# Optimization experiments

Hardware: AMD Instinct MI355X
Metric: run time of the kernel (lower is better)

The kernel has to match this reference:

```python
import jax, jax.numpy as jnp
import numpy as np

A = 512   # input channels
B = 32    # number of capsule types
H4 = 16   # h*h pose dims per capsule


def setup_inputs() -> dict:
    key = jax.random.key(0)
    k1, k2, k3, k4, k5 = jax.random.split(key, 5)
    # Input feature map [N, A, H, W]
    x = jax.random.normal(k1, (64, A, 32, 32), dtype=jnp.float32)
    # Fused weights: B parallel 1x1 convs concatenated along out-channel dim.
    # Pose convs: B x Conv2d(A -> 16, k=1) -> [B*16, A]; activation convs: B x Conv2d(A -> 1) -> [B, A]
    bound = 1.0 / np.sqrt(A)  # PyTorch Conv2d default init range
    W_pose = jax.random.uniform(k2, (B * H4, A), minval=-bound, maxval=bound, dtype=jnp.float32)
    b_pose = jax.random.uniform(k3, (B * H4,), minval=-bound, maxval=bound, dtype=jnp.float32)
    W_act = jax.random.uniform(k4, (B, A), minval=-bound, maxval=bound, dtype=jnp.float32)
    b_act = jax.random.uniform(k5, (B,), minval=-bound, maxval=bound, dtype=jnp.float32)
    return {"x": x, "W_pose": W_pose, "b_pose": b_pose, "W_act": W_act, "b_act": b_act}


def reference(x, W_pose, b_pose, W_act, b_act):
    # 1x1 conv == channel contraction; fuse all 2*B tiny convs into two GEMMs.
    # poses: [N, B*16, H, W]
    poses = jnp.einsum('nahw,oa->nohw', x, W_pose) + b_pose[None, :, None, None]
    # activations: sigmoid([N, B, H, W])
    activations = jax.nn.sigmoid(jnp.einsum('nahw,oa->nohw', x, W_act) + b_act[None, :, None, None])
    return poses, activations
```

## Files before the change

### kernel.cpp

```cpp
#include <hip/hip_runtime.h>
#include <hip/hip_bf16.h>


typedef __attribute__((ext_vector_type(8))) short short8;
typedef __attribute__((ext_vector_type(4))) float f32x4;

#define A_CH   512
#define HW     1024
#define N_B    64
#define O_POSE 512
#define O_ACT  32
#define O_TOT  544
#define TILE   128
#define BK     32

__device__ __forceinline__ unsigned pack_bf16x2(float lo, float hi) {
    __hip_bfloat162 h = __float22bfloat162_rn(make_float2(lo, hi));
    return *reinterpret_cast<unsigned*>(&h);
}

__global__ __launch_bounds__(256) void caps_fused_gemm(
    const float* __restrict__ x,
    const float* __restrict__ Wp,
    const float* __restrict__ bp,
    const float* __restrict__ Wa,
    const float* __restrict__ ba,
    float* __restrict__ out)
{
    __shared__ __align__(16) short ldsA[TILE * BK];
    __shared__ __align__(16) short ldsB[TILE * BK];

    const int tid = threadIdx.x;
    const int n   = blockIdx.z;
    const int o0  = blockIdx.y * TILE;
    const int m0  = blockIdx.x * TILE;

    const float* xn = x + (size_t)n * A_CH * HW + m0;

    const int bm  = tid & 127;
    const int bkh = (tid >> 7) * 16;

    float4 a_reg[4];
    float  b_reg[4][4];

    auto load_tiles = [&](int k0) {
#pragma unroll
        for (int c = 0; c < 4; ++c) {
            int lin = tid + 256 * c;
            int o = lin >> 3, kc = lin & 7;
            int R = o0 + o;
            float4 v = make_float4(0.f, 0.f, 0.f, 0.f);
            if (R < O_POSE)     v = *(const float4*)(Wp + (size_t)R * A_CH + k0 + kc * 4);
            else if (R < O_TOT) v = *(const float4*)(Wa + (size_t)(R - O_POSE) * A_CH + k0 + kc * 4);
            a_reg[c] = v;
        }
#pragma unroll
        for (int c = 0; c < 4; ++c) {
            int kb = k0 + bkh + c * 4;
#pragma unroll
            for (int j = 0; j < 4; ++j)
                b_reg[c][j] = xn[(size_t)(kb + j) * HW + bm];
        }
    };

    auto store_tiles = [&]() {
#pragma unroll
        for (int c = 0; c < 4; ++c) {
            int lin = tid + 256 * c;
            int o = lin >> 3, kc = lin & 7;
            int kx = (kc * 4) ^ (8 * ((o >> 1) & 3));
            uint2 p;
            p.x = pack_bf16x2(a_reg[c].x, a_reg[c].y);
            p.y = pack_bf16x2(a_reg[c].z, a_reg[c].w);
            *(uint2*)&ldsA[o * BK + kx] = p;
        }
#pragma unroll
        for (int c = 0; c < 4; ++c) {
            int kloc = bkh + c * 4;
            int kx = kloc ^ (8 * ((bm >> 1) & 3));
            uint2 p;
            p.x = pack_bf16x2(b_reg[c][0], b_reg[c][1]);
            p.y = pack_bf16x2(b_reg[c][2], b_reg[c][3]);
            *(uint2*)&ldsB[bm * BK + kx] = p;
        }
    };

    const int lane = tid & 63;
    const int w    = tid >> 6;
    const int wo   = (w >> 1) * 64;
    const int wm   = (w & 1) * 64;
    const int l16  = lane & 15;
    const int g    = lane >> 4;

    f32x4 acc[4][4] = {};

    load_tiles(0);

    for (int it = 0; it < A_CH / BK; ++it) {
        __syncthreads();
        store_tiles();
        __syncthreads();
        if (it + 1 < A_CH / BK) load_tiles((it + 1) * BK);

        short8 aF[4], bF[4];
#pragma unroll
        for (int f = 0; f < 4; ++f) {
            int r  = wo + f * 16 + l16;
            int kx = (g * 8) ^ (8 * ((r >> 1) & 3));
            aF[f] = *(const short8*)&ldsA[r * BK + kx];
            int cC  = wm + f * 16 + l16;
            int kxb = (g * 8) ^ (8 * ((cC >> 1) & 3));
            bF[f] = *(const short8*)&ldsB[cC * BK + kxb];
        }
#pragma unroll
        for (int fo = 0; fo < 4; ++fo)
#pragma unroll
            for (int fm = 0; fm < 4; ++fm)
                acc[fo][fm] = __builtin_amdgcn_mfma_f32_16x16x32_bf16(
                    aF[fo], bF[fm], acc[fo][fm], 0, 0, 0);
    }

    float* actOut = out + (size_t)N_B * O_POSE * HW;
    const size_t poseN = (size_t)n * O_POSE * HW;
    const size_t actN  = (size_t)n * O_ACT * HW;
#pragma unroll
    for (int fo = 0; fo < 4; ++fo) {
#pragma unroll
        for (int i = 0; i < 4; ++i) {
            int R = o0 + wo + fo * 16 + g * 4 + i;
            if (R >= O_TOT) continue;
            if (R < O_POSE) {
                float bias = bp[R];
#pragma unroll
                for (int fm = 0; fm < 4; ++fm) {
                    int cc = m0 + wm + fm * 16 + l16;
                    out[poseN + (size_t)R * HW + cc] = acc[fo][fm][i] + bias;
                }
            } else {
                float bias = ba[R - O_POSE];
#pragma unroll
                for (int fm = 0; fm < 4; ++fm) {
                    int cc = m0 + wm + fm * 16 + l16;
                    float v = acc[fo][fm][i] + bias;
                    actOut[actN + (size_t)(R - O_POSE) * HW + cc] = 1.0f / (1.0f + __expf(-v));
                }
            }
        }
    }
}

extern "C" void kernel_launch(void* const* d_in, const int* in_sizes, int n_in,
                              void* d_out, int out_size, void* d_ws, size_t ws_size,
                              hipStream_t stream) {
    (void)in_sizes; (void)n_in; (void)d_ws; (void)ws_size; (void)out_size;
    const float* x  = (const float*)d_in[0];
    const float* Wp = (const float*)d_in[1];
    const float* bp = (const float*)d_in[2];
    const float* Wa = (const float*)d_in[3];
    const float* ba = (const float*)d_in[4];
    dim3 grid(HW / TILE, (O_TOT + TILE - 1) / TILE, N_B);
    caps_fused_gemm<<<grid, dim3(256), 0, stream>>>(x, Wp, bp, Wa, ba, (float*)d_out);
}
```

Before: 311.0 us.

## Double-buffer LDS, widen spatial tile to 256, and use nontemporal output stores

After: 291.3 us. 1.07x faster.

```diff
diff --git a/kernel.cpp b/kernel.cpp
--- a/kernel.cpp
+++ b/kernel.cpp
@@ -11,15 +11,17 @@
 #define O_POSE 512
 #define O_ACT  32
 #define O_TOT  544
-#define TILE   128
+#define TO     128
+#define TM     256
 #define BK     32
+#define NIT    (A_CH / BK)
 
-__device__ __forceinline__ unsigned pack_bf16x2(float lo, float hi) {
+__device__ __forceinline__ unsigned pk(float lo, float hi) {
     __hip_bfloat162 h = __float22bfloat162_rn(make_float2(lo, hi));
     return *reinterpret_cast<unsigned*>(&h);
 }
 
-__global__ __launch_bounds__(256) void caps_fused_gemm(
+__global__ __launch_bounds__(512, 4) void caps_fused_gemm(
     const float* __restrict__ x,
     const float* __restrict__ Wp,
     const float* __restrict__ bp,
@@ -27,97 +29,97 @@
     const float* __restrict__ ba,
     float* __restrict__ out)
 {
-    __shared__ __align__(16) short ldsA[TILE * BK];
-    __shared__ __align__(16) short ldsB[TILE * BK];
+    __shared__ __align__(16) short ldsA[2][TO * BK];
+    __shared__ __align__(16) short ldsB[2][TM * BK];
 
     const int tid = threadIdx.x;
     const int n   = blockIdx.z;
-    const int o0  = blockIdx.y * TILE;
-    const int m0  = blockIdx.x * TILE;
+    const int o0  = blockIdx.y * TO;
+    const int m0  = blockIdx.x * TM;
 
     const float* xn = x + (size_t)n * A_CH * HW + m0;
 
-    const int bm  = tid & 127;
-    const int bkh = (tid >> 7) * 16;
+    const int ao = tid >> 2;
+    const int ak = (tid & 3) * 8;
+    const float* arow = nullptr;
+    {
+        int R = o0 + ao;
+        if (R < O_POSE)     arow = Wp + (size_t)R * A_CH + ak;
+        else if (R < O_TOT) arow = Wa + (size_t)(R - O_POSE) * A_CH + ak;
+    }
+    const int bm = tid & 255;
+    const int bk = (tid >> 8) * 16;
+    const float* bbase = xn + (size_t)bk * HW + bm;
 
-    float4 a_reg[4];
-    float  b_reg[4][4];
+    float4 a0, a1;
+    float  breg[16];
 
     auto load_tiles = [&](int k0) {
-#pragma unroll
-        for (int c = 0; c < 4; ++c) {
-            int lin = tid + 256 * c;
-            int o = lin >> 3, kc = lin & 7;
-            int R = o0 + o;
-            float4 v = make_float4(0.f, 0.f, 0.f, 0.f);
-            if (R < O_POSE)     v = *(const float4*)(Wp + (size_t)R * A_CH + k0 + kc * 4);
-            else if (R < O_TOT) v = *(const float4*)(Wa + (size_t)(R - O_POSE) * A_CH + k0 + kc * 4);
-            a_reg[c] = v;
+        if (arow) {
+            a0 = *(const float4*)(arow + k0);
+            a1 = *(const float4*)(arow + k0 + 4);
+        } else {
+            a0 = make_float4(0.f, 0.f, 0.f, 0.f);
+            a1 = a0;
         }
 #pragma unroll
-        for (int c = 0; c < 4; ++c) {
-            int kb = k0 + bkh + c * 4;
-#pragma unroll
-            for (int j = 0; j < 4; ++j)
-                b_reg[c][j] = xn[(size_t)(kb + j) * HW + bm];
-        }
+        for (int j = 0; j < 16; ++j)
+            breg[j] = bbase[(size_t)(k0 + j) * HW];
     };
 
-    auto store_tiles = [&]() {
+    const int aswz = 8 * ((ao >> 1) & 3);
+    const int bswz = 8 * ((bm >> 1) & 3);
+
+    auto store_tiles = [&](int buf) {
+        short8 av;
+        ((unsigned*)&av)[0] = pk(a0.x, a0.y);
+        ((unsigned*)&av)[1] = pk(a0.z, a0.w);
+        ((unsigned*)&av)[2] = pk(a1.x, a1.y);
+        ((unsigned*)&av)[3] = pk(a1.z, a1.w);
+        *(short8*)&ldsA[buf][ao * BK + (ak ^ aswz)] = av;
+
+        short8 b0, b1;
 #pragma unroll
-        for (int c = 0; c < 4; ++c) {
-            int lin = tid + 256 * c;
-            int o = lin >> 3, kc = lin & 7;
-            int kx = (kc * 4) ^ (8 * ((o >> 1) & 3));
-            uint2 p;
-            p.x = pack_bf16x2(a_reg[c].x, a_reg[c].y);
-            p.y = pack_bf16x2(a_reg[c].z, a_reg[c].w);
-            *(uint2*)&ldsA[o * BK + kx] = p;
+        for (int j = 0; j < 4; ++j) {
+            ((unsigned*)&b0)[j] = pk(breg[2 * j], breg[2 * j + 1]);
+            ((unsigned*)&b1)[j] = pk(breg[8 + 2 * j], breg[9 + 2 * j]);
         }
-#pragma unroll
-        for (int c = 0; c < 4; ++c) {
-            int kloc = bkh + c * 4;
-            int kx = kloc ^ (8 * ((bm >> 1) & 3));
-            uint2 p;
-            p.x = pack_bf16x2(b_reg[c][0], b_reg[c][1]);
-            p.y = pack_bf16x2(b_reg[c][2], b_reg[c][3]);
-            *(uint2*)&ldsB[bm * BK + kx] = p;
-        }
+        *(short8*)&ldsB[buf][bm * BK + (bk ^ bswz)]       = b0;
+        *(short8*)&ldsB[buf][bm * BK + ((bk + 8) ^ bswz)] = b1;
     };
 
     const int lane = tid & 63;
     const int w    = tid >> 6;
-    const int wo   = (w >> 1) * 64;
-    const int wm   = (w & 1) * 64;
+    const int wo   = (w >> 2) * 64;
+    const int wm   = (w & 3) * 64;
     const int l16  = lane & 15;
     const int g    = lane >> 4;
 
     f32x4 acc[4][4] = {};
 
     load_tiles(0);
+    store_tiles(0);
+    __syncthreads();
 
-    for (int it = 0; it < A_CH / BK; ++it) {
-        __syncthreads();
-        store_tiles();
-        __syncthreads();
-        if (it + 1 < A_CH / BK) load_tiles((it + 1) * BK);
-
+    for (int it = 0; it < NIT; ++it) {
+        const int cur = it & 1;
         short8 aF[4], bF[4];
 #pragma unroll
         for (int f = 0; f < 4; ++f) {
-            int r  = wo + f * 16 + l16;
-            int kx = (g * 8) ^ (8 * ((r >> 1) & 3));
-            aF[f] = *(const short8*)&ldsA[r * BK + kx];
-            int cC  = wm + f * 16 + l16;
-            int kxb = (g * 8) ^ (8 * ((cC >> 1) & 3));
-            bF[f] = *(const short8*)&ldsB[cC * BK + kxb];
+            int r = wo + f * 16 + l16;
+            aF[f] = *(const short8*)&ldsA[cur][r * BK + ((g * 8) ^ (8 * ((r >> 1) & 3)))];
+            int c = wm + f * 16 + l16;
+            bF[f] = *(const short8*)&ldsB[cur][c * BK + ((g * 8) ^ (8 * ((c >> 1) & 3)))];
         }
+        if (it + 1 < NIT) load_tiles((it + 1) * BK);
 #pragma unroll
         for (int fo = 0; fo < 4; ++fo)
 #pragma unroll
             for (int fm = 0; fm < 4; ++fm)
                 acc[fo][fm] = __builtin_amdgcn_mfma_f32_16x16x32_bf16(
                     aF[fo], bF[fm], acc[fo][fm], 0, 0, 0);
+        if (it + 1 < NIT) store_tiles(cur ^ 1);
+        __syncthreads();
     }
 
     float* actOut = out + (size_t)N_B * O_POSE * HW;
@@ -134,7 +136,8 @@
 #pragma unroll
                 for (int fm = 0; fm < 4; ++fm) {
                     int cc = m0 + wm + fm * 16 + l16;
-                    out[poseN + (size_t)R * HW + cc] = acc[fo][fm][i] + bias;
+                    __builtin_nontemporal_store(acc[fo][fm][i] + bias,
+                                                &out[poseN + (size_t)R * HW + cc]);
                 }
             } else {
                 float bias = ba[R - O_POSE];
@@ -142,7 +145,8 @@
                 for (int fm = 0; fm < 4; ++fm) {
                     int cc = m0 + wm + fm * 16 + l16;
                     float v = acc[fo][fm][i] + bias;
-                    actOut[actN + (size_t)(R - O_POSE) * HW + cc] = 1.0f / (1.0f + __expf(-v));
+                    __builtin_nontemporal_store(1.0f / (1.0f + __expf(-v)),
+                                                &actOut[actN + (size_t)(R - O_POSE) * HW + cc]);
                 }
             }
         }
@@ -158,6 +162,6 @@
     const float* bp = (const float*)d_in[2];
     const float* Wa = (const float*)d_in[3];
     const float* ba = (const float*)d_in[4];
-    dim3 grid(HW / TILE, (O_TOT + TILE - 1) / TILE, N_B);
-    caps_fused_gemm<<<grid, dim3(256), 0, stream>>>(x, Wp, bp, Wa, ba, (float*)d_out);
+    dim3 grid(HW / TM, (O_TOT + TO - 1) / TO, N_B);
+    caps_fused_gemm<<<grid, dim3(512), 0, stream>>>(x, Wp, bp, Wa, ba, (float*)d_out);
 }
```
